# Optimization experiments

Hardware: AMD Instinct MI355X
Metric: run time of the kernel (lower is better)

## Reference

```python
import jax, jax.numpy as jnp
import numpy as np


def setup_inputs() -> dict:
    key = jax.random.key(0)
    k1, k2, k3, k4 = jax.random.split(key, 4)
    B, N, M, D = 4, 4096, 4096, 64
    x = jax.random.normal(k1, (B, N, D), dtype=jnp.float32)
    y = jax.random.normal(k2, (B, M, D), dtype=jnp.float32)
    mu = jax.random.normal(k3, (D, 1), dtype=jnp.float32)
    logs2diag = jax.random.normal(k4, (D,), dtype=jnp.float32) * 0.1
    return {"x": x, "y": y, "mu": mu, "logs2diag": logs2diag}


def reference(x, y, mu, logs2diag):
    # Diagonal scaling: x_ = x @ diag(exp(logs2diag)**0.5) == x * s_sqrt (broadcast)
    s_sqrt = jnp.exp(0.5 * logs2diag)  # [D]
    x_ = x * s_sqrt  # [B,N,D]
    y_ = y * s_sqrt  # [B,M,D]
    # cos term: M = x@mu - (y@mu)^T  -> [B,N,M]
    m_x = jnp.einsum('bnd,dk->bnk', x, mu)  # [B,N,1]
    m_y = jnp.einsum('bmd,dk->bmk', y, mu)  # [B,M,1]
    Mdiff = m_x - jnp.swapaxes(m_y, 1, 2)   # [B,N,M]
    # squared euclidean distance without sqrt (exp(-0.5*cdist^2))
    x2 = jnp.sum(x_ * x_, axis=-1, keepdims=True)      # [B,N,1]
    y2 = jnp.sum(y_ * y_, axis=-1, keepdims=True)      # [B,M,1]
    xy = jnp.einsum('bnd,bmd->bnm', x_, y_)            # [B,N,M]
    sqd = jnp.maximum(x2 + jnp.swapaxes(y2, 1, 2) - 2.0 * xy, 0.0)
    return jnp.cos(Mdiff) * jnp.exp(-0.5 * sqd)
```

## Files before the change

### kernel.cpp

```cpp
#include <hip/hip_runtime.h>
#include <math.h>

typedef __attribute__((ext_vector_type(8))) short short8;
typedef __attribute__((ext_vector_type(4))) float f32x4;

constexpr int D  = 64;
constexpr int BT = 64;

__device__ inline float fastcos_rev(float r) {
#if __has_builtin(__builtin_amdgcn_cosf)
    return __builtin_amdgcn_cosf(r);
#else
    return __cosf(r * 6.283185307179586f);
#endif
}
__device__ inline float fastsin_rev(float r) {
#if __has_builtin(__builtin_amdgcn_sinf)
    return __builtin_amdgcn_sinf(r);
#else
    return __sinf(r * 6.283185307179586f);
#endif
}

__device__ inline void split8(const float* v, short8& hi, short8& lo) {
    #pragma unroll
    for (int j = 0; j < 8; ++j) {
        unsigned u = __builtin_bit_cast(unsigned, v[j]);
        hi[j] = (short)(u >> 16);
        float hf = __builtin_bit_cast(float, u & 0xffff0000u);
        float r  = v[j] - hf;
        lo[j] = (short)(__builtin_bit_cast(unsigned, r) >> 16);
    }
}

__global__ __launch_bounds__(256) void prep_kernel(
    const float* __restrict__ x, const float* __restrict__ y,
    const float* __restrict__ mu, const float* __restrict__ ls2,
    unsigned short* __restrict__ xh, unsigned short* __restrict__ xl,
    unsigned short* __restrict__ yh, unsigned short* __restrict__ yl,
    float4* __restrict__ xst, float4* __restrict__ yst,
    int BN, int BM)
{
    __shared__ float ss[D], sm[D];
    const int t = threadIdx.x;
    if (t < D) { ss[t] = __expf(0.5f * ls2[t]); sm[t] = mu[t]; }
    __syncthreads();

    const int row = blockIdx.x * 256 + t;
    if (row >= BN + BM) return;

    const float* src;
    unsigned short *ph, *pl;
    float4* pst;
    int r;
    if (row < BN) { r = row;      src = x + (size_t)r * D; ph = xh; pl = xl; pst = xst; }
    else          { r = row - BN; src = y + (size_t)r * D; ph = yh; pl = yl; pst = yst; }

    float v[D];
    float h = 0.f, m = 0.f;
    #pragma unroll
    for (int d = 0; d < D; d += 4) {
        float4 u = *(const float4*)(src + d);
        m += u.x * sm[d] + u.y * sm[d+1] + u.z * sm[d+2] + u.w * sm[d+3];
        u.x *= ss[d]; u.y *= ss[d+1]; u.z *= ss[d+2]; u.w *= ss[d+3];
        h += u.x * u.x + u.y * u.y + u.z * u.z + u.w * u.w;
        v[d] = u.x; v[d+1] = u.y; v[d+2] = u.z; v[d+3] = u.w;
    }

    constexpr float INV2PI = 0.15915494309189535f;
    float rr = m * INV2PI;
    rr -= floorf(rr);
    pst[r] = (float4){0.5f * h, fastcos_rev(rr), fastsin_rev(rr), 0.f};

    const size_t tileBase = (size_t)(r >> 4) * 1024;
    const int rl = r & 15;
    #pragma unroll
    for (int sl = 0; sl < 8; ++sl) {
        short8 hi, lo;
        split8(&v[sl * 8], hi, lo);
        *(short8*)(ph + tileBase + (size_t)(sl * 16 + rl) * 8) = hi;
        *(short8*)(pl + tileBase + (size_t)(sl * 16 + rl) * 8) = lo;
    }
}

__global__ __launch_bounds__(256) void main_kernel(
    const unsigned short* __restrict__ xh, const unsigned short* __restrict__ xl,
    const unsigned short* __restrict__ yh, const unsigned short* __restrict__ yl,
    const float4* __restrict__ xst, const float4* __restrict__ yst,
    float* __restrict__ out, int N, int M)
{
    __shared__ float4 stA[BT], stB[BT];

    const int b  = blockIdx.z;
    const int n0 = blockIdx.y * BT;
    const int m0 = blockIdx.x * BT;
    const int t  = threadIdx.x;

    if (t < BT)           stA[t] = xst[(size_t)b * N + n0 + t];
    else if (t < 2 * BT)  stB[t - BT] = yst[(size_t)b * M + m0 + (t - BT)];
    __syncthreads();

    const int w = t >> 6, lane = t & 63;
    const int wr = w >> 1, wc = w & 1;
    const int l15 = lane & 15, lg = lane >> 4;

    f32x4 acc[2][2];
    #pragma unroll
    for (int i = 0; i < 2; ++i)
        #pragma unroll
        for (int j = 0; j < 2; ++j)
            acc[i][j] = (f32x4){0.f, 0.f, 0.f, 0.f};

    const size_t tA0 = ((size_t)(b * N + n0) >> 4) + wr * 2;
    const size_t tB0 = ((size_t)(b * M + m0) >> 4) + wc * 2;

    #pragma unroll
    for (int kc = 0; kc < 2; ++kc) {
        const size_t koff = (size_t)kc * 512 + (size_t)lane * 8;
        short8 ah[2], al[2], bh[2], bl[2];
        #pragma unroll
        for (int i = 0; i < 2; ++i) {
            const size_t o = (tA0 + i) * 1024 + koff;
            ah[i] = *(const short8*)(xh + o);
            al[i] = *(const short8*)(xl + o);
        }
        #pragma unroll
        for (int j = 0; j < 2; ++j) {
            const size_t o = (tB0 + j) * 1024 + koff;
            bh[j] = *(const short8*)(yh + o);
            bl[j] = *(const short8*)(yl + o);
        }
        #pragma unroll
        for (int i = 0; i < 2; ++i)
            #pragma unroll
            for (int j = 0; j < 2; ++j) {
                acc[i][j] = __builtin_amdgcn_mfma_f32_16x16x32_bf16(ah[i], bh[j], acc[i][j], 0, 0, 0);
                acc[i][j] = __builtin_amdgcn_mfma_f32_16x16x32_bf16(ah[i], bl[j], acc[i][j], 0, 0, 0);
                acc[i][j] = __builtin_amdgcn_mfma_f32_16x16x32_bf16(al[i], bh[j], acc[i][j], 0, 0, 0);
            }
    }

    float hyv[2], cyv[2], syv[2];
    #pragma unroll
    for (int j = 0; j < 2; ++j) {
        float4 s = stB[wc * 32 + j * 16 + l15];
        hyv[j] = s.x; cyv[j] = s.y; syv[j] = s.z;
    }
    #pragma unroll
    for (int i = 0; i < 2; ++i) {
        #pragma unroll
        for (int q = 0; q < 4; ++q) {
            const int nl = wr * 32 + i * 16 + lg * 4 + q;
            const float4 sa = stA[nl];
            float* orow = out + ((size_t)(b * N + n0 + nl)) * (size_t)M + m0 + wc * 32;
            #pragma unroll
            for (int j = 0; j < 2; ++j) {
                const float e  = (acc[i][j][q] - sa.x) - hyv[j];
                const float cv = sa.y * cyv[j] + sa.z * syv[j];
                __builtin_nontemporal_store(cv * __expf(e), &orow[j * 16 + l15]);
            }
        }
    }
}

constexpr int FTILE = 64;
constexpr int FPAD  = 68;
__global__ __launch_bounds__(256) void fallback_kernel(
    const float* __restrict__ x, const float* __restrict__ y,
    const float* __restrict__ mu, const float* __restrict__ ls2,
    float* __restrict__ out, int N, int M)
{
    __shared__ float xs[FTILE][FPAD];
    __shared__ float ys[FTILE][FPAD];
    __shared__ float musc[D];
    __shared__ float sx2[FTILE], smx[FTILE], sy2[FTILE], smy[FTILE];

    const int b  = blockIdx.z;
    const int n0 = blockIdx.y * FTILE;
    const int m0 = blockIdx.x * FTILE;
    const int t  = threadIdx.x;
    const int cc = t & 15, rr = t >> 4, c4 = cc * 4;

    const float s0 = __expf(0.5f * ls2[c4+0]);
    const float s1 = __expf(0.5f * ls2[c4+1]);
    const float s2 = __expf(0.5f * ls2[c4+2]);
    const float s3 = __expf(0.5f * ls2[c4+3]);
    const float* xb = x + ((size_t)b * N + n0) * D;
    const float* yb = y + ((size_t)b * M + m0) * D;

    #pragma unroll
    for (int r = 0; r < 4; ++r) {
        const int row = rr * 4 + r;
        const float4 vx = *(const float4*)(xb + row * D + c4);
        const float4 vy = *(const float4*)(yb + row * D + c4);
        xs[row][c4+0] = vx.x * s0; xs[row][c4+1] = vx.y * s1;
        xs[row][c4+2] = vx.z * s2; xs[row][c4+3] = vx.w * s3;
        ys[row][c4+0] = vy.x * s0; ys[row][c4+1] = vy.y * s1;
        ys[row][c4+2] = vy.z * s2; ys[row][c4+3] = vy.w * s3;
    }
    if (t < D) musc[t] = mu[t] * __expf(-0.5f * ls2[t]);
    __syncthreads();

    if (t < 64) {
        float a2 = 0.f, am = 0.f;
        #pragma unroll
        for (int d4 = 0; d4 < D; d4 += 4) {
            const float4 v = *(const float4*)&xs[t][d4];
            const float4 m4 = *(const float4*)&musc[d4];
            a2 += v.x*v.x + v.y*v.y + v.z*v.z + v.w*v.w;
            am += v.x*m4.x + v.y*m4.y + v.z*m4.z + v.w*m4.w;
        }
        sx2[t] = a2; smx[t] = am;
    } else if (t < 128) {
        const int r2 = t - 64;
        float a2 = 0.f, am = 0.f;
        #pragma unroll
        for (int d4 = 0; d4 < D; d4 += 4) {
            const float4 v = *(const float4*)&ys[r2][d4];
            const float4 m4 = *(const float4*)&musc[d4];
            a2 += v.x*v.x + v.y*v.y + v.z*v.z + v.w*v.w;
            am += v.x*m4.x + v.y*m4.y + v.z*m4.z + v.w*m4.w;
        }
        sy2[r2] = a2; smy[r2] = am;
    }
    __syncthreads();

    const int tx = t & 15, ty = t >> 4;
    float acc[4][4] = {};
    #pragma unroll
    for (int d = 0; d < D; d += 4) {
        float4 a4[4], b4[4];
        #pragma unroll
        for (int i = 0; i < 4; ++i) a4[i] = *(const float4*)&xs[ty + 16*i][d];
        #pragma unroll
        for (int j = 0; j < 4; ++j) b4[j] = *(const float4*)&ys[tx + 16*j][d];
        #pragma unroll
        for (int i = 0; i < 4; ++i)
            #pragma unroll
            for (int j = 0; j < 4; ++j) {
                acc[i][j] += a4[i].x*b4[j].x + a4[i].y*b4[j].y
                           + a4[i].z*b4[j].z + a4[i].w*b4[j].w;
            }
    }

    constexpr float INV2PI = 0.15915494309189535f;
    #pragma unroll
    for (int i = 0; i < 4; ++i) {
        const int nl = ty + 16*i;
        float* orow = out + ((size_t)(b * N + n0 + nl)) * (size_t)M + m0;
        const float x2v = sx2[nl], mxv = smx[nl];
        #pragma unroll
        for (int j = 0; j < 4; ++j) {
            const int ml = tx + 16*j;
            float sqd = fmaxf(x2v + sy2[ml] - 2.0f*acc[i][j], 0.0f);
            float r = (mxv - smy[ml]) * INV2PI;
            r -= floorf(r);
            orow[ml] = fastcos_rev(r) * __expf(-0.5f * sqd);
        }
    }
}

extern "C" void kernel_launch(void* const* d_in, const int* in_sizes, int n_in,
                              void* d_out, int out_size, void* d_ws, size_t ws_size,
                              hipStream_t stream)
{
    const float* x   = (const float*)d_in[0];
    const float* y   = (const float*)d_in[1];
    const float* mu  = (const float*)d_in[2];
    const float* ls2 = (const float*)d_in[3];
    float* out = (float*)d_out;

    const int Dd = in_sizes[3];
    const long long BN = in_sizes[0] / Dd;
    const long long BM = in_sizes[1] / Dd;
    const int B = (int)((BN * BM) / (long long)out_size);
    const int N = (int)(BN / B);
    const int M = (int)(BM / B);

    const size_t need = (size_t)(BN + BM) * D * 2 * 2
                      + (size_t)(BN + BM) * sizeof(float4);

    if (ws_size >= need && (N % BT) == 0 && (M % BT) == 0) {
        unsigned short* xh = (unsigned short*)d_ws;
        unsigned short* xl = xh + (size_t)BN * D;
        unsigned short* yh = xl + (size_t)BN * D;
        unsigned short* yl = yh + (size_t)BM * D;
        float4* xst = (float4*)(yl + (size_t)BM * D);
        float4* yst = xst + BN;

        const int rows = (int)(BN + BM);
        hipLaunchKernelGGL(prep_kernel, dim3((rows + 255) / 256), dim3(256), 0, stream,
                           x, y, mu, ls2, xh, xl, yh, yl, xst, yst, (int)BN, (int)BM);
        hipLaunchKernelGGL(main_kernel, dim3(M / BT, N / BT, B), dim3(256), 0, stream,
                           xh, xl, yh, yl, xst, yst, out, N, M);
    } else {
        hipLaunchKernelGGL(fallback_kernel, dim3(M / FTILE, N / FTILE, B), dim3(256), 0, stream,
                           x, y, mu, ls2, out, N, M);
    }
}
```

Before: 74.49 us.

## Retile main kernel to 32x512 blocks with XCD-aware swizzle and vector stores

Changes the output tile from 64x64 to 32 rows by 512 columns with 8 waves per block, each wave covering 64 columns. The MFMA operands are swapped so each lane holds four consecutive output columns, which allows 16-byte nontemporal stores instead of scalar ones. A block-index swizzle over 8 groups maps neighbouring tiles to the same XCD for L2 locality. The aim is more efficient write bandwidth on this output-store-bound kernel, at the cost of a stricter divisibility condition for the fast path.

```diff
diff --git a/kernel.cpp b/kernel.cpp
--- a/kernel.cpp
+++ b/kernel.cpp
@@ -4,8 +4,9 @@
 typedef __attribute__((ext_vector_type(8))) short short8;
 typedef __attribute__((ext_vector_type(4))) float f32x4;
 
-constexpr int D  = 64;
-constexpr int BT = 64;
+constexpr int D    = 64;
+constexpr int BT_N = 32;
+constexpr int BT_M = 512;
 
 __device__ inline float fastcos_rev(float r) {
 #if __has_builtin(__builtin_amdgcn_cosf)
@@ -83,41 +84,44 @@
     }
 }
 
-__global__ __launch_bounds__(256) void main_kernel(
+__global__ __launch_bounds__(512) void main_kernel(
     const unsigned short* __restrict__ xh, const unsigned short* __restrict__ xl,
     const unsigned short* __restrict__ yh, const unsigned short* __restrict__ yl,
     const float4* __restrict__ xst, const float4* __restrict__ yst,
-    float* __restrict__ out, int N, int M)
+    float* __restrict__ out, int N, int M, int tiles_n, int tiles_m, int nblocks)
 {
-    __shared__ float4 stA[BT], stB[BT];
-
-    const int b  = blockIdx.z;
-    const int n0 = blockIdx.y * BT;
-    const int m0 = blockIdx.x * BT;
-    const int t  = threadIdx.x;
-
-    if (t < BT)           stA[t] = xst[(size_t)b * N + n0 + t];
-    else if (t < 2 * BT)  stB[t - BT] = yst[(size_t)b * M + m0 + (t - BT)];
+    __shared__ float4 stA[BT_N], stB[BT_M];
+
+    const int bid  = blockIdx.x;
+    const int tile = (bid & 7) * (nblocks >> 3) + (bid >> 3);
+    const int tpb  = tiles_n * tiles_m;
+    const int b    = tile / tpb;
+    const int rr   = tile % tpb;
+    const int n0   = (rr / tiles_m) * BT_N;
+    const int m0   = (rr % tiles_m) * BT_M;
+
+    const int t = threadIdx.x;
+    if (t < BT_N) stA[t] = xst[(size_t)b * N + n0 + t];
+    stB[t] = yst[(size_t)b * M + m0 + t];
     __syncthreads();
 
     const int w = t >> 6, lane = t & 63;
-    const int wr = w >> 1, wc = w & 1;
     const int l15 = lane & 15, lg = lane >> 4;
 
-    f32x4 acc[2][2];
+    f32x4 acc[2][4];
     #pragma unroll
     for (int i = 0; i < 2; ++i)
         #pragma unroll
-        for (int j = 0; j < 2; ++j)
+        for (int j = 0; j < 4; ++j)
             acc[i][j] = (f32x4){0.f, 0.f, 0.f, 0.f};
 
-    const size_t tA0 = ((size_t)(b * N + n0) >> 4) + wr * 2;
-    const size_t tB0 = ((size_t)(b * M + m0) >> 4) + wc * 2;
+    const size_t tA0 = ((size_t)(b * N + n0) >> 4);
+    const size_t tB0 = ((size_t)(b * M + m0) >> 4) + w * 4;
 
     #pragma unroll
     for (int kc = 0; kc < 2; ++kc) {
         const size_t koff = (size_t)kc * 512 + (size_t)lane * 8;
-        short8 ah[2], al[2], bh[2], bl[2];
+        short8 ah[2], al[2], bh[4], bl[4];
         #pragma unroll
         for (int i = 0; i < 2; ++i) {
             const size_t o = (tA0 + i) * 1024 + koff;
@@ -125,7 +129,7 @@
             al[i] = *(const short8*)(xl + o);
         }
         #pragma unroll
-        for (int j = 0; j < 2; ++j) {
+        for (int j = 0; j < 4; ++j) {
             const size_t o = (tB0 + j) * 1024 + koff;
             bh[j] = *(const short8*)(yh + o);
             bl[j] = *(const short8*)(yl + o);
@@ -133,32 +137,32 @@
         #pragma unroll
         for (int i = 0; i < 2; ++i)
             #pragma unroll
-            for (int j = 0; j < 2; ++j) {
-                acc[i][j] = __builtin_amdgcn_mfma_f32_16x16x32_bf16(ah[i], bh[j], acc[i][j], 0, 0, 0);
-                acc[i][j] = __builtin_amdgcn_mfma_f32_16x16x32_bf16(ah[i], bl[j], acc[i][j], 0, 0, 0);
-                acc[i][j] = __builtin_amdgcn_mfma_f32_16x16x32_bf16(al[i], bh[j], acc[i][j], 0, 0, 0);
+            for (int j = 0; j < 4; ++j) {
+                acc[i][j] = __builtin_amdgcn_mfma_f32_16x16x32_bf16(bh[j], ah[i], acc[i][j], 0, 0, 0);
+                acc[i][j] = __builtin_amdgcn_mfma_f32_16x16x32_bf16(bh[j], al[i], acc[i][j], 0, 0, 0);
+                acc[i][j] = __builtin_amdgcn_mfma_f32_16x16x32_bf16(bl[j], ah[i], acc[i][j], 0, 0, 0);
             }
     }
 
-    float hyv[2], cyv[2], syv[2];
-    #pragma unroll
-    for (int j = 0; j < 2; ++j) {
-        float4 s = stB[wc * 32 + j * 16 + l15];
-        hyv[j] = s.x; cyv[j] = s.y; syv[j] = s.z;
-    }
+    float4 sa[2];
+    #pragma unroll
+    for (int i = 0; i < 2; ++i) sa[i] = stA[i * 16 + l15];
+
     #pragma unroll
     for (int i = 0; i < 2; ++i) {
-        #pragma unroll
-        for (int q = 0; q < 4; ++q) {
-            const int nl = wr * 32 + i * 16 + lg * 4 + q;
-            const float4 sa = stA[nl];
-            float* orow = out + ((size_t)(b * N + n0 + nl)) * (size_t)M + m0 + wc * 32;
+        const int n = n0 + i * 16 + l15;
+        float* orow = out + ((size_t)(b * N + n)) * (size_t)M + m0 + w * 64;
+        #pragma unroll
+        for (int j = 0; j < 4; ++j) {
+            f32x4 r;
             #pragma unroll
-            for (int j = 0; j < 2; ++j) {
-                const float e  = (acc[i][j][q] - sa.x) - hyv[j];
-                const float cv = sa.y * cyv[j] + sa.z * syv[j];
-                __builtin_nontemporal_store(cv * __expf(e), &orow[j * 16 + l15]);
+            for (int q = 0; q < 4; ++q) {
+                const float4 sb = stB[w * 64 + j * 16 + lg * 4 + q];
+                const float e  = (acc[i][j][q] - sa[i].x) - sb.x;
+                const float cv = sa[i].y * sb.y + sa[i].z * sb.z;
+                r[q] = cv * __expf(e);
             }
+            __builtin_nontemporal_store(r, (f32x4*)(orow + j * 16 + lg * 4));
         }
     }
 }
@@ -280,7 +284,10 @@
     const size_t need = (size_t)(BN + BM) * D * 2 * 2
                       + (size_t)(BN + BM) * sizeof(float4);
 
-    if (ws_size >= need && (N % BT) == 0 && (M % BT) == 0) {
+    const int tiles_n = N / BT_N, tiles_m = M / BT_M;
+    const int nblocks = B * tiles_n * tiles_m;
+
+    if (ws_size >= need && (N % BT_N) == 0 && (M % BT_M) == 0 && (nblocks % 8) == 0) {
         unsigned short* xh = (unsigned short*)d_ws;
         unsigned short* xl = xh + (size_t)BN * D;
         unsigned short* yh = xl + (size_t)BN * D;
@@ -291,8 +298,8 @@
         const int rows = (int)(BN + BM);
         hipLaunchKernelGGL(prep_kernel, dim3((rows + 255) / 256), dim3(256), 0, stream,
                            x, y, mu, ls2, xh, xl, yh, yl, xst, yst, (int)BN, (int)BM);
-        hipLaunchKernelGGL(main_kernel, dim3(M / BT, N / BT, B), dim3(256), 0, stream,
-                           xh, xl, yh, yl, xst, yst, out, N, M);
+        hipLaunchKernelGGL(main_kernel, dim3(nblocks), dim3(512), 0, stream,
+                           xh, xl, yh, yl, xst, yst, out, N, M, tiles_n, tiles_m, nblocks);
     } else {
         hipLaunchKernelGGL(fallback_kernel, dim3(M / FTILE, N / FTILE, B), dim3(256), 0, stream,
                            x, y, mu, ls2, out, N, M);
```

Result: slower. 87.60 us (+17.6%).

## Widen main tile along M with register-reused A fragments and double-buffered B loads

Applied to the files above, without the earlier changes.

Each main-kernel block now covers 64 rows by 512 columns. It loads the A hi/lo fragments and per-row stats once, then loops over eight 64-column subtiles, prefetching the next B fragments while the current one computes and stores. The prep kernel splits each row across 8 threads and combines partial sums with shuffles, which gives it more parallelism. The output store switches from nontemporal to regular stores, and the larger tile cuts the block count eightfold, which may reduce occupancy on a 4096x4096x4 output.

```diff
diff --git a/kernel.cpp b/kernel.cpp
--- a/kernel.cpp
+++ b/kernel.cpp
@@ -4,8 +4,10 @@
 typedef __attribute__((ext_vector_type(8))) short short8;
 typedef __attribute__((ext_vector_type(4))) float f32x4;
 
-constexpr int D  = 64;
-constexpr int BT = 64;
+constexpr int D    = 64;
+constexpr int BT_N = 64;
+constexpr int BT_M = 512;
+constexpr int NSUB = 8;
 
 __device__ inline float fastcos_rev(float r) {
 #if __has_builtin(__builtin_amdgcn_cosf)
@@ -46,7 +48,9 @@
     if (t < D) { ss[t] = __expf(0.5f * ls2[t]); sm[t] = mu[t]; }
     __syncthreads();
 
-    const int row = blockIdx.x * 256 + t;
+    const int gid = blockIdx.x * 256 + t;
+    const int row = gid >> 3;
+    const int sub = gid & 7;
     if (row >= BN + BM) return;
 
     const float* src;
@@ -56,30 +60,90 @@
     if (row < BN) { r = row;      src = x + (size_t)r * D; ph = xh; pl = xl; pst = xst; }
     else          { r = row - BN; src = y + (size_t)r * D; ph = yh; pl = yl; pst = yst; }
 
-    float v[D];
-    float h = 0.f, m = 0.f;
-    #pragma unroll
-    for (int d = 0; d < D; d += 4) {
-        float4 u = *(const float4*)(src + d);
-        m += u.x * sm[d] + u.y * sm[d+1] + u.z * sm[d+2] + u.w * sm[d+3];
-        u.x *= ss[d]; u.y *= ss[d+1]; u.z *= ss[d+2]; u.w *= ss[d+3];
-        h += u.x * u.x + u.y * u.y + u.z * u.z + u.w * u.w;
-        v[d] = u.x; v[d+1] = u.y; v[d+2] = u.z; v[d+3] = u.w;
-    }
-
-    constexpr float INV2PI = 0.15915494309189535f;
-    float rr = m * INV2PI;
-    rr -= floorf(rr);
-    pst[r] = (float4){0.5f * h, fastcos_rev(rr), fastsin_rev(rr), 0.f};
-
-    const size_t tileBase = (size_t)(r >> 4) * 1024;
-    const int rl = r & 15;
-    #pragma unroll
-    for (int sl = 0; sl < 8; ++sl) {
-        short8 hi, lo;
-        split8(&v[sl * 8], hi, lo);
-        *(short8*)(ph + tileBase + (size_t)(sl * 16 + rl) * 8) = hi;
-        *(short8*)(pl + tileBase + (size_t)(sl * 16 + rl) * 8) = lo;
+    const int k0 = sub * 8;
+    float4 u0 = *(const float4*)(src + k0);
+    float4 u1 = *(const float4*)(src + k0 + 4);
+    const float4 m0 = *(const float4*)&sm[k0];
+    const float4 m1 = *(const float4*)&sm[k0 + 4];
+    const float4 s0 = *(const float4*)&ss[k0];
+    const float4 s1 = *(const float4*)&ss[k0 + 4];
+
+    float m = u0.x*m0.x + u0.y*m0.y + u0.z*m0.z + u0.w*m0.w
+            + u1.x*m1.x + u1.y*m1.y + u1.z*m1.z + u1.w*m1.w;
+    u0.x *= s0.x; u0.y *= s0.y; u0.z *= s0.z; u0.w *= s0.w;
+    u1.x *= s1.x; u1.y *= s1.y; u1.z *= s1.z; u1.w *= s1.w;
+    float h = u0.x*u0.x + u0.y*u0.y + u0.z*u0.z + u0.w*u0.w
+            + u1.x*u1.x + u1.y*u1.y + u1.z*u1.z + u1.w*u1.w;
+
+    m += __shfl_xor(m, 1); m += __shfl_xor(m, 2); m += __shfl_xor(m, 4);
+    h += __shfl_xor(h, 1); h += __shfl_xor(h, 2); h += __shfl_xor(h, 4);
+
+    if (sub == 0) {
+        constexpr float INV2PI = 0.15915494309189535f;
+        float rr = m * INV2PI;
+        rr -= floorf(rr);
+        pst[r] = (float4){0.5f * h, fastcos_rev(rr), fastsin_rev(rr), 0.f};
+    }
+
+    float v[8] = {u0.x, u0.y, u0.z, u0.w, u1.x, u1.y, u1.z, u1.w};
+    short8 hi, lo;
+    split8(v, hi, lo);
+    const size_t o = (size_t)(r >> 4) * 1024 + (size_t)(sub * 16 + (r & 15)) * 8;
+    *(short8*)(ph + o) = hi;
+    *(short8*)(pl + o) = lo;
+}
+
+__device__ __forceinline__ void load_b(
+    short8 (&bh)[2][2], short8 (&bl)[2][2],
+    const unsigned short* __restrict__ ybh, const unsigned short* __restrict__ ybl,
+    int st)
+{
+    #pragma unroll
+    for (int kc = 0; kc < 2; ++kc)
+        #pragma unroll
+        for (int j = 0; j < 2; ++j) {
+            const size_t o = (size_t)st * 4096 + j * 1024 + kc * 512;
+            bh[kc][j] = *(const short8*)(ybh + o);
+            bl[kc][j] = *(const short8*)(ybl + o);
+        }
+}
+
+__device__ __forceinline__ void compute_store(
+    const short8 (&ah)[2][2], const short8 (&al)[2][2],
+    const short8 (&bh)[2][2], const short8 (&bl)[2][2],
+    const float4* __restrict__ stB,
+    const float (&sax)[2][4], const float (&say)[2][4], const float (&saz)[2][4],
+    float* __restrict__ outb, int M, int st, int wc, int l15)
+{
+    f32x4 acc[2][2];
+    #pragma unroll
+    for (int i = 0; i < 2; ++i)
+        #pragma unroll
+        for (int j = 0; j < 2; ++j)
+            acc[i][j] = (f32x4){0.f, 0.f, 0.f, 0.f};
+
+    #pragma unroll
+    for (int kc = 0; kc < 2; ++kc)
+        #pragma unroll
+        for (int i = 0; i < 2; ++i)
+            #pragma unroll
+            for (int j = 0; j < 2; ++j) {
+                acc[i][j] = __builtin_amdgcn_mfma_f32_16x16x32_bf16(ah[kc][i], bh[kc][j], acc[i][j], 0, 0, 0);
+                acc[i][j] = __builtin_amdgcn_mfma_f32_16x16x32_bf16(ah[kc][i], bl[kc][j], acc[i][j], 0, 0, 0);
+                acc[i][j] = __builtin_amdgcn_mfma_f32_16x16x32_bf16(al[kc][i], bh[kc][j], acc[i][j], 0, 0, 0);
+            }
+
+    #pragma unroll
+    for (int j = 0; j < 2; ++j) {
+        const float4 sb = stB[st * 64 + wc * 32 + j * 16 + l15];
+        #pragma unroll
+        for (int i = 0; i < 2; ++i)
+            #pragma unroll
+            for (int q = 0; q < 4; ++q) {
+                const float e  = (acc[i][j][q] - sax[i][q]) - sb.x;
+                const float cv = say[i][q] * sb.y + saz[i][q] * sb.z;
+                outb[(size_t)(i * 16 + q) * M + st * 64 + j * 16] = cv * __expf(e);
+            }
     }
 }
 
@@ -89,77 +153,59 @@
     const float4* __restrict__ xst, const float4* __restrict__ yst,
     float* __restrict__ out, int N, int M)
 {
-    __shared__ float4 stA[BT], stB[BT];
+    __shared__ float4 stA[BT_N], stB[BT_M];
 
     const int b  = blockIdx.z;
-    const int n0 = blockIdx.y * BT;
-    const int m0 = blockIdx.x * BT;
+    const int n0 = blockIdx.y * BT_N;
+    const int m0 = blockIdx.x * BT_M;
     const int t  = threadIdx.x;
 
-    if (t < BT)           stA[t] = xst[(size_t)b * N + n0 + t];
-    else if (t < 2 * BT)  stB[t - BT] = yst[(size_t)b * M + m0 + (t - BT)];
+    stB[t]       = yst[(size_t)b * M + m0 + t];
+    stB[t + 256] = yst[(size_t)b * M + m0 + 256 + t];
+    if (t < BT_N) stA[t] = xst[(size_t)b * N + n0 + t];
     __syncthreads();
 
     const int w = t >> 6, lane = t & 63;
     const int wr = w >> 1, wc = w & 1;
     const int l15 = lane & 15, lg = lane >> 4;
 
-    f32x4 acc[2][2];
+    const size_t tA0 = (((size_t)b * N + n0) >> 4) + wr * 2;
+    const size_t tB0 = (((size_t)b * M + m0) >> 4) + wc * 2;
+    const unsigned short* xbh = xh + tA0 * 1024 + (size_t)lane * 8;
+    const unsigned short* xbl = xl + tA0 * 1024 + (size_t)lane * 8;
+    const unsigned short* ybh = yh + tB0 * 1024 + (size_t)lane * 8;
+    const unsigned short* ybl = yl + tB0 * 1024 + (size_t)lane * 8;
+
+    short8 ah[2][2], al[2][2];
+    #pragma unroll
+    for (int kc = 0; kc < 2; ++kc)
+        #pragma unroll
+        for (int i = 0; i < 2; ++i) {
+            ah[kc][i] = *(const short8*)(xbh + i * 1024 + kc * 512);
+            al[kc][i] = *(const short8*)(xbl + i * 1024 + kc * 512);
+        }
+
+    float sax[2][4], say[2][4], saz[2][4];
     #pragma unroll
     for (int i = 0; i < 2; ++i)
         #pragma unroll
-        for (int j = 0; j < 2; ++j)
-            acc[i][j] = (f32x4){0.f, 0.f, 0.f, 0.f};
-
-    const size_t tA0 = ((size_t)(b * N + n0) >> 4) + wr * 2;
-    const size_t tB0 = ((size_t)(b * M + m0) >> 4) + wc * 2;
-
-    #pragma unroll
-    for (int kc = 0; kc < 2; ++kc) {
-        const size_t koff = (size_t)kc * 512 + (size_t)lane * 8;
-        short8 ah[2], al[2], bh[2], bl[2];
-        #pragma unroll
-        for (int i = 0; i < 2; ++i) {
-            const size_t o = (tA0 + i) * 1024 + koff;
-            ah[i] = *(const short8*)(xh + o);
-            al[i] = *(const short8*)(xl + o);
-        }
-        #pragma unroll
-        for (int j = 0; j < 2; ++j) {
-            const size_t o = (tB0 + j) * 1024 + koff;
-            bh[j] = *(const short8*)(yh + o);
-            bl[j] = *(const short8*)(yl + o);
-        }
-        #pragma unroll
-        for (int i = 0; i < 2; ++i)
-            #pragma unroll
-            for (int j = 0; j < 2; ++j) {
-                acc[i][j] = __builtin_amdgcn_mfma_f32_16x16x32_bf16(ah[i], bh[j], acc[i][j], 0, 0, 0);
-                acc[i][j] = __builtin_amdgcn_mfma_f32_16x16x32_bf16(ah[i], bl[j], acc[i][j], 0, 0, 0);
-                acc[i][j] = __builtin_amdgcn_mfma_f32_16x16x32_bf16(al[i], bh[j], acc[i][j], 0, 0, 0);
-            }
-    }
-
-    float hyv[2], cyv[2], syv[2];
-    #pragma unroll
-    for (int j = 0; j < 2; ++j) {
-        float4 s = stB[wc * 32 + j * 16 + l15];
-        hyv[j] = s.x; cyv[j] = s.y; syv[j] = s.z;
-    }
-    #pragma unroll
-    for (int i = 0; i < 2; ++i) {
-        #pragma unroll
         for (int q = 0; q < 4; ++q) {
-            const int nl = wr * 32 + i * 16 + lg * 4 + q;
-            const float4 sa = stA[nl];
-            float* orow = out + ((size_t)(b * N + n0 + nl)) * (size_t)M + m0 + wc * 32;
-            #pragma unroll
-            for (int j = 0; j < 2; ++j) {
-                const float e  = (acc[i][j][q] - sa.x) - hyv[j];
-                const float cv = sa.y * cyv[j] + sa.z * syv[j];
-                __builtin_nontemporal_store(cv * __expf(e), &orow[j * 16 + l15]);
-            }
-        }
+            const float4 v = stA[wr * 32 + i * 16 + lg * 4 + q];
+            sax[i][q] = v.x; say[i][q] = v.y; saz[i][q] = v.z;
+        }
+
+    float* outb = out + ((size_t)b * N + n0 + wr * 32 + lg * 4) * (size_t)M
+                + m0 + wc * 32 + l15;
+
+    short8 bh0[2][2], bl0[2][2], bh1[2][2], bl1[2][2];
+    load_b(bh0, bl0, ybh, ybl, 0);
+    #pragma unroll
+    for (int st = 0; st < NSUB; st += 2) {
+        if (st + 1 < NSUB) load_b(bh1, bl1, ybh, ybl, st + 1);
+        compute_store(ah, al, bh0, bl0, stB, sax, say, saz, outb, M, st, wc, l15);
+        if (st + 2 < NSUB) load_b(bh0, bl0, ybh, ybl, st + 2);
+        if (st + 1 < NSUB)
+            compute_store(ah, al, bh1, bl1, stB, sax, say, saz, outb, M, st + 1, wc, l15);
     }
 }
 
@@ -280,7 +326,7 @@
     const size_t need = (size_t)(BN + BM) * D * 2 * 2
                       + (size_t)(BN + BM) * sizeof(float4);
 
-    if (ws_size >= need && (N % BT) == 0 && (M % BT) == 0) {
+    if (ws_size >= need && (N % BT_N) == 0 && (M % BT_M) == 0) {
         unsigned short* xh = (unsigned short*)d_ws;
         unsigned short* xl = xh + (size_t)BN * D;
         unsigned short* yh = xl + (size_t)BN * D;
@@ -288,10 +334,10 @@
         float4* xst = (float4*)(yl + (size_t)BM * D);
         float4* yst = xst + BN;
 
-        const int rows = (int)(BN + BM);
-        hipLaunchKernelGGL(prep_kernel, dim3((rows + 255) / 256), dim3(256), 0, stream,
+        const long long rows8 = (BN + BM) * 8;
+        hipLaunchKernelGGL(prep_kernel, dim3((int)((rows8 + 255) / 256)), dim3(256), 0, stream,
                            x, y, mu, ls2, xh, xl, yh, yl, xst, yst, (int)BN, (int)BM);
-        hipLaunchKernelGGL(main_kernel, dim3(M / BT, N / BT, B), dim3(256), 0, stream,
+        hipLaunchKernelGGL(main_kernel, dim3(M / BT_M, N / BT_N, B), dim3(256), 0, stream,
                            xh, xl, yh, yl, xst, yst, out, N, M);
     } else {
         hipLaunchKernelGGL(fallback_kernel, dim3(M / FTILE, N / FTILE, B), dim3(256), 0, stream,
```

Measured after the change: 66.55 us. -10.7%, faster.
